# Optimization experiments

Hardware: AMD Instinct MI355X
Metric: run time of the kernel (lower is better)

Reference implementation:

```python
import jax, jax.numpy as jnp
import numpy as np

B, C, H, W = 4, 128, 128, 128
E, K, HID = 11, 6, 512  # num_experts, active_experts, 4*dim


def setup_inputs() -> dict:
    key = jax.random.key(0)
    ks = jax.random.split(key, 5)
    return {
        "x": jax.random.normal(ks[0], (B, C, H, W), jnp.float32),
        "gate_w": jax.random.normal(ks[1], (E, C), jnp.float32) * 0.02,
        "gate_b": jnp.zeros((E,), jnp.float32),
        "w1": jax.random.normal(ks[2], (E, HID, C), jnp.float32) * 0.02,
        "b1": jnp.zeros((E, HID), jnp.float32),
        "w2": jax.random.normal(ks[3], (E, C, HID), jnp.float32) * 0.02,
        "b2": jnp.zeros((E, C), jnp.float32),
    }


def reference(x, gate_w, gate_b, w1, b1, w2, b2):
    n_experts = gate_w.shape[0]
    k = K  # active_experts
    # channels-last for per-pixel routing / 1x1-conv-as-matmul
    xcl = jnp.transpose(x, (0, 2, 3, 1))  # [B,H,W,C]
    # --- router (1x1 conv gate + softmax over experts + top-k) ---
    logits = jnp.einsum('bhwc,ec->bhwe', xcl, gate_w) + gate_b
    scores = jax.nn.softmax(logits, axis=-1)            # [B,H,W,E]
    topk_p, topk_i = jax.lax.top_k(scores, k)           # [B,H,W,K]
    topk_p = topk_p / topk_p.sum(axis=-1, keepdims=True)
    # scatter routing weights into dense per-expert mask (indices distinct)
    onehot = jax.nn.one_hot(topk_i, n_experts, dtype=x.dtype)  # [B,H,W,K,E]
    mask = jnp.einsum('bhwke,bhwk->bhwe', onehot, topk_p)      # [B,H,W,E]
    # --- dense expert compute, masked accumulate (as in original loop) ---
    acc = jnp.zeros_like(xcl)
    for e in range(n_experts):
        h = jax.nn.gelu(jnp.einsum('bhwc,dc->bhwd', xcl, w1[e]) + b1[e],
                        approximate=False)  # torch GELU is exact erf form
        oe = jnp.einsum('bhwd,cd->bhwc', h, w2[e]) + b2[e]
        acc = acc + mask[..., e:e + 1] * oe
    y = x + jnp.transpose(acc, (0, 3, 1, 2))  # back to NCHW
    # --- load-balancing aux loss ---
    mean_prob = scores.mean(axis=(0, 1, 2))            # [E]
    mean_load = onehot.sum(axis=3).mean(axis=(0, 1, 2))  # binary mask mean, [E]
    aux_loss = n_experts * jnp.sum(mean_prob * mean_load)
    return (y, aux_loss)
```

## Files before the change

### kernel.cpp

```cpp
#include <hip/hip_runtime.h>
#include <stdint.h>

#define C_   128
#define HW_  16384
#define CHW_ (C_*HW_)
#define N_   65536
#define E_   11
#define K_   6
#define HID_ 512

typedef __attribute__((ext_vector_type(8))) _Float16 half8;
typedef __attribute__((ext_vector_type(2))) _Float16 h2;
typedef __attribute__((ext_vector_type(2))) __fp16 fp16v2;
typedef __attribute__((ext_vector_type(16))) float float16v;
typedef __attribute__((ext_vector_type(2))) unsigned uint2v;

#define GLD(g, s) __builtin_amdgcn_global_load_lds( \
    (const __attribute__((address_space(1))) unsigned int*)(uintptr_t)(g), \
    (__attribute__((address_space(3))) unsigned int*)(unsigned int)(uintptr_t)(s), 16, 0, 0)

__device__ __forceinline__ h2 pkrtz(float a, float b){
  union { fp16v2 f; h2 h; } u;
  u.f = __builtin_amdgcn_cvt_pkrtz(a, b);
  return u.h;
}
__device__ __forceinline__ h2 gelu2h(h2 v, h2 wr2){
  h2 u = v * v;
  h2 s = u * (h2)(_Float16)(-0.00076957f) + (h2)(_Float16)(0.0147811f);
  s = s * u + (h2)(_Float16)(-0.126434f);
  s = s * u + (h2)(_Float16)(0.795742f);
  h2 p = v * s;
  h2 phi = p * (h2)(_Float16)(0.5f) + (h2)(_Float16)(0.5f);
  return v * wr2 * phi;
}
__device__ __forceinline__ void pswap32(unsigned &a, unsigned &b){
#if __has_builtin(__builtin_amdgcn_permlane32_swap)
  uint2v r = __builtin_amdgcn_permlane32_swap(a, b, false, false);
  a = r.x; b = r.y;
#else
  asm volatile("v_permlane32_swap_b32 %0, %1" : "+v"(a), "+v"(b));
#endif
}

__global__ __launch_bounds__(256) void k_convert(const float* __restrict__ w1,
                                                 const float* __restrict__ w2,
                                                 const float* __restrict__ b1,
                                                 unsigned short* __restrict__ wimg,
                                                 unsigned short* __restrict__ b1h,
                                                 float* __restrict__ auxsum){
  int t = blockIdx.x * 256 + threadIdx.x;
  if (t < 23) auxsum[t] = 0.0f;
  if (t >= 185856) return;
  if (t >= 180224){
    int t2 = t - 180224;
    int rec = t2 >> 5, j5 = t2 & 31;
    int hi = j5 >> 4, j = j5 & 15;
    int e = rec >> 4, hc = rec & 15;
    int row = (j & 3) + 8 * (j >> 2) + 4 * hi;
    union { _Float16 h; unsigned short u; } cv;
    cv.h = (_Float16)b1[e * 512 + hc * 32 + row];
    b1h[rec * 32 + j5] = cv.u;
    return;
  }
  const float* src;
  size_t dst;
  if (t < 90112){
    int e = t >> 13, hid = (t >> 4) & 511, c8 = t & 15;
    src = w1 + (size_t)t * 8;
    int rec = e * 16 + (hid >> 5);
    int kc = c8 >> 1, half = c8 & 1;
    int l = (hid & 31) | (half << 5);
    dst = (size_t)rec * 8192 + kc * 512 + l * 8;
  } else {
    int u = t - 90112;
    int e = u >> 13, cc = (u >> 6) & 127, hd8 = u & 63;
    src = w2 + (size_t)u * 8;
    int rec = e * 16 + (hd8 >> 2);
    int kc2 = (hd8 >> 1) & 1, half = hd8 & 1, ct = cc >> 5;
    int l = (cc & 31) | (half << 5);
    dst = (size_t)rec * 8192 + 4096 + (ct * 2 + kc2) * 512 + l * 8;
  }
  float4 a = *(const float4*)src, b = *(const float4*)(src + 4);
  union { _Float16 h[8]; uint4 v; } u4;
  u4.h[0] = (_Float16)a.x; u4.h[1] = (_Float16)a.y;
  u4.h[2] = (_Float16)a.z; u4.h[3] = (_Float16)a.w;
  u4.h[4] = (_Float16)b.x; u4.h[5] = (_Float16)b.y;
  u4.h[6] = (_Float16)b.z; u4.h[7] = (_Float16)b.w;
  *(uint4*)(wimg + dst) = u4.v;
}

__global__ __launch_bounds__(512, 2) void k_ffn(const float* __restrict__ x,
                                                const float* __restrict__ gw,
                                                const float* __restrict__ gb,
                                                float* __restrict__ mask,
                                                const unsigned short* __restrict__ wimg,
                                                const unsigned short* __restrict__ b1h,
                                                const float* __restrict__ b2,
                                                float* __restrict__ auxsum,
                                                float* __restrict__ y){
  __shared__ unsigned char smem[65536];
  __shared__ int b2f;
  int tid = threadIdx.x;
  int w = tid >> 6, l = tid & 63;
  int l31 = l & 31, hi = l >> 5;
  int hi4 = hi * 4;
  int pix0 = blockIdx.x * 256;
  int off = (blockIdx.x % 11) * 16;
  const unsigned char* wimgB = (const unsigned char*)wimg;
  const unsigned char* b1hB  = (const unsigned char*)b1h;

  if (tid == 0) b2f = 0;

  half8 Xf[8];

  {
    float* tt  = (float*)smem;
    float* g   = (float*)(smem + 33280);
    float* gbs = (float*)(smem + 38912);
    float* ap  = (float*)(smem + 38976);
    float* al  = (float*)(smem + 39040);

    for (int i = tid; i < E_ * C_; i += 512) g[i] = gw[i];
    if (tid < E_){ gbs[tid] = gb[tid]; ap[tid] = 0.f; al[tid] = 0.f; }

    int myrr = w >> 1;
    #pragma unroll 1
    for (int rr = 0; rr < 4; ++rr){
      int pixc = pix0 + rr * 64;
      const float* xb = x + (size_t)(pixc >> 14) * CHW_ + (pixc & 16383);
      __syncthreads();
      #pragma unroll
      for (int it = 0; it < 4; ++it){
        int flat = it * 512 + tid;
        int c = flat >> 4, p4 = (flat & 15) << 2;
        float4 v = *(const float4*)(xb + (size_t)c * HW_ + p4);
        tt[(p4 + 0) * 130 + c] = v.x;
        tt[(p4 + 1) * 130 + c] = v.y;
        tt[(p4 + 2) * 130 + c] = v.z;
        tt[(p4 + 3) * 130 + c] = v.w;
      }
      __syncthreads();
      if (myrr == rr){
        const float2* trow = (const float2*)(tt + (32 * (w & 1) + l31) * 130 + hi * 8);
        #pragma unroll
        for (int kc = 0; kc < 8; ++kc){
          union { unsigned u[4]; half8 s; } cv;
          #pragma unroll
          for (int m = 0; m < 4; ++m){
            float2 f = trow[kc * 8 + m];
            union { h2 h; unsigned uu; } pv;
            pv.h = pkrtz(f.x, f.y);
            cv.u[m] = pv.uu;
          }
          Xf[kc] = cv.s;
        }
      }
      if (tid < 256){
        int p = tid >> 2, t4 = tid & 3;
        float lg[E_];
        #pragma unroll
        for (int e = 0; e < E_; ++e) lg[e] = (t4 == 0) ? gbs[e] : 0.f;
        const float2* ttrow = (const float2*)(tt + p * 130 + t4 * 32);
        #pragma unroll 4
        for (int j2 = 0; j2 < 16; ++j2){
          float2 xv = ttrow[j2];
          #pragma unroll
          for (int e = 0; e < E_; ++e){
            float2 gv = *(const float2*)(g + e * C_ + t4 * 32 + j2 * 2);
            lg[e] = fmaf(xv.x, gv.x, lg[e]);
            lg[e] = fmaf(xv.y, gv.y, lg[e]);
          }
        }
        #pragma unroll
        for (int e = 0; e < E_; ++e){
          lg[e] += __shfl_xor(lg[e], 1, 64);
          lg[e] += __shfl_xor(lg[e], 2, 64);
        }
        float mx = lg[0];
        #pragma unroll
        for (int e = 1; e < E_; ++e) mx = fmaxf(mx, lg[e]);
        float pr[E_]; float s = 0.f;
        #pragma unroll
        for (int e = 0; e < E_; ++e){ pr[e] = expf(lg[e] - mx); s += pr[e]; }
        float inv = 1.0f / s;
        #pragma unroll
        for (int e = 0; e < E_; ++e) pr[e] *= inv;

        unsigned selmask = 0; float wsum = 0.f;
        for (int k = 0; k < K_; ++k){
          float bv = -1.f; int bi = 0;
          #pragma unroll
          for (int e = 0; e < E_; ++e){
            bool better = (((selmask >> e) & 1u) == 0u) && (pr[e] > bv);
            bv = better ? pr[e] : bv;
            bi = better ? e : bi;
          }
          selmask |= 1u << bi; wsum += bv;
        }
        float invw = 1.0f / wsum;
        if (t4 == 0){
          int pix = pixc + p;
          #pragma unroll
          for (int e = 0; e < E_; ++e){
            bool sel = (selmask >> e) & 1u;
            mask[(size_t)pix * E_ + e] = sel ? pr[e] * invw : 0.f;
            atomicAdd(&ap[e], pr[e]);
            if (sel) atomicAdd(&al[e], 1.0f);
          }
        }
      }
    }
    __syncthreads();
    if (tid < E_){
      atomicAdd(&auxsum[tid], ap[tid]);
      atomicAdd(&auxsum[E_ + tid], al[tid]);
    }
  }

  uint4 bhA[4], bhB[4];
  const size_t mrow = (size_t)(pix0 + w * 32 + l31) * 11;

  {
    #pragma unroll
    for (int k = 0; k < 2; ++k){
      int rec = off + k;
      const unsigned char* gs = wimgB + (size_t)rec * 16384 + w * 2048 + l * 16;
      unsigned char* dst = smem + k * 16384 + w * 2048;
      GLD(gs, dst);
      GLD(gs + 1024, dst + 1024);
    }
    #pragma unroll
    for (int k = 0; k < 2; ++k){
      const unsigned char* bp = b1hB + (off + k) * 64 + hi * 32;
      bhA[2 * k]     = *(const uint4*)(bp);
      bhA[2 * k + 1] = *(const uint4*)(bp + 16);
    }
  }
  float wrn = mask[mrow + (off >> 4)];
  __syncthreads();

  float16v facc[4];
  #pragma unroll
  for (int ct = 0; ct < 4; ++ct) facc[ct] = (float16v)0.0f;
  h2 wr2 = (h2)(_Float16)0.0f;

#define REC_BODY(WB, BH0, BH1)                                                      \
  {                                                                                 \
    float16v hacc_ = (float16v)0.0f;                                                \
    _Pragma("unroll")                                                               \
    for (int kc_ = 0; kc_ < 8; ++kc_){                                              \
      half8 a_ = *(const half8*)((WB) + kc_ * 1024 + l * 16);                       \
      hacc_ = __builtin_amdgcn_mfma_f32_32x32x16_f16(a_, Xf[kc_], hacc_, 0, 0, 0);  \
    }                                                                               \
    union { uint4 v[2]; h2 h[8]; } bu_;                                             \
    bu_.v[0] = BH0; bu_.v[1] = BH1;                                                 \
    unsigned pd_[8];                                                                \
    _Pragma("unroll")                                                               \
    for (int k_ = 0; k_ < 8; ++k_){                                                 \
      h2 v_ = pkrtz(hacc_[2 * k_], hacc_[2 * k_ + 1]);                              \
      v_ = v_ + bu_.h[k_];                                                          \
      union { h2 h; unsigned u; } g_;                                               \
      g_.h = gelu2h(v_, wr2);                                                       \
      pd_[k_] = g_.u;                                                               \
    }                                                                               \
    pswap32(pd_[0], pd_[2]); pswap32(pd_[1], pd_[3]);                               \
    pswap32(pd_[4], pd_[6]); pswap32(pd_[5], pd_[7]);                               \
    union { unsigned u[4]; half8 s; } cv0_, cv1_;                                   \
    cv0_.u[0] = pd_[0]; cv0_.u[1] = pd_[1]; cv0_.u[2] = pd_[2]; cv0_.u[3] = pd_[3]; \
    cv1_.u[0] = pd_[4]; cv1_.u[1] = pd_[5]; cv1_.u[2] = pd_[6]; cv1_.u[3] = pd_[7]; \
    _Pragma("unroll")                                                               \
    for (int ct_ = 0; ct_ < 4; ++ct_){                                              \
      half8 a0_ = *(const half8*)((WB) + 8192 + (ct_ * 2 + 0) * 1024 + l * 16);     \
      half8 a1_ = *(const half8*)((WB) + 8192 + (ct_ * 2 + 1) * 1024 + l * 16);     \
      facc[ct_] = __builtin_amdgcn_mfma_f32_32x32x16_f16(a0_, cv0_.s, facc[ct_], 0, 0, 0); \
      facc[ct_] = __builtin_amdgcn_mfma_f32_32x32x16_f16(a1_, cv1_.s, facc[ct_], 0, 0, 0); \
    }                                                                               \
  }

#define SUPER_BODY(J, BHC, BHL)                                                     \
  {                                                                                 \
    asm volatile("s_waitcnt vmcnt(4)" ::: "memory");                                \
    __builtin_amdgcn_s_barrier();                                                   \
    __builtin_amdgcn_sched_barrier(0);                                              \
         \
    {                                                                               \
      unsigned char* dbuf_ = smem + ((((J) + 1) & 1) << 15);                        \
      _Pragma("unroll")                                                             \
      for (int k_ = 0; k_ < 2; ++k_){                                               \
        int rn_ = 2 * (J) + 2 + k_ + off; if (rn_ >= 176) rn_ -= 176;               \
        const unsigned char* gs_ = wimgB + (size_t)rn_ * 16384 + w * 2048 + l * 16; \
        unsigned char* dst_ = dbuf_ + k_ * 16384 + w * 2048;                        \
        GLD(gs_, dst_);                                                             \
        GLD(gs_ + 1024, dst_ + 1024);                                               \
      }                                                                             \
      __builtin_amdgcn_sched_barrier(0);                                            \
      _Pragma("unroll")                                                             \
      for (int k_ = 0; k_ < 2; ++k_){                                               \
        int rn_ = 2 * (J) + 2 + k_ + off; if (rn_ >= 176) rn_ -= 176;               \
        const unsigned char* bp_ = b1hB + rn_ * 64 + hi * 32;                       \
        BHL[2 * k_]     = *(const uint4*)(bp_);                                     \
        BHL[2 * k_ + 1] = *(const uint4*)(bp_ + 16);                                \
      }                                                                             \
    }                                                                               \
    __builtin_amdgcn_sched_barrier(0);                                              \
    if (((J) & 7) == 0){           \
      _Float16 wh_ = (_Float16)wrn;                                                 \
      wr2 = (h2){wh_, wh_};                                                         \
      int rn_ = 2 * (J) + 16 + off; if (rn_ >= 176) rn_ -= 176;                     \
      wrn = mask[mrow + (rn_ >> 4)];                                                \
    }                                                                               \
    const unsigned char* wb_ = smem + (((J) & 1) << 15);                            \
    REC_BODY(wb_, BHC[0], BHC[1]);                                                  \
    REC_BODY(wb_ + 16384, BHC[2], BHC[3]);                                          \
  }

  #pragma unroll 1
  for (int jj = 0; jj < 44; ++jj){
    SUPER_BODY(2 * jj,     bhA, bhB);
    SUPER_BODY(2 * jj + 1, bhB, bhA);
  }
#undef SUPER_BODY
#undef REC_BODY

  __syncthreads();
  float* lds_t = (float*)smem;
  float* b2t   = (float*)(smem + 17408);
  for (int idx = tid; idx < 1536; idx += 512){
    int cc = idx / 12, ee = idx - cc * 12;
    float v = (ee < 11) ? b2[ee * 128 + cc] : 0.f;
    b2t[idx] = v;
    if (v != 0.f) atomicOr(&b2f, 1);
  }
  __syncthreads();
  int b2nz = b2f;

  #pragma unroll 1
  for (int h = 0; h < 8; ++h){
    __syncthreads();
    if (w == h){
      #pragma unroll
      for (int ct = 0; ct < 4; ++ct)
        #pragma unroll
        for (int r = 0; r < 16; ++r)
          lds_t[(ct * 32 + (r & 3) + 8 * (r >> 2) + hi4) * 33 + l31] = facc[ct][r];
    }
    __syncthreads();
    int c = tid >> 2, p8 = (tid & 3) << 3;
    int pixg = pix0 + h * 32 + p8;
    size_t base = (size_t)(pixg >> 14) * CHW_ + (size_t)c * HW_ + (pixg & 16383);
    float av[8];
    #pragma unroll
    for (int k = 0; k < 8; ++k) av[k] = lds_t[c * 33 + p8 + k];
    if (b2nz){
      #pragma unroll
      for (int k = 0; k < 8; ++k){
        const float* mr = mask + (size_t)(pixg + k) * 11;
        #pragma unroll
        for (int e = 0; e < 11; ++e) av[k] = fmaf(mr[e], b2t[c * 12 + e], av[k]);
      }
    }
    float4 xv0 = *(const float4*)(x + base);
    float4 xv1 = *(const float4*)(x + base + 4);
    float4 o0 = {av[0] + xv0.x, av[1] + xv0.y, av[2] + xv0.z, av[3] + xv0.w};
    float4 o1 = {av[4] + xv1.x, av[5] + xv1.y, av[6] + xv1.z, av[7] + xv1.w};
    *(float4*)(y + base) = o0;
    *(float4*)(y + base + 4) = o1;
  }
}

__global__ __launch_bounds__(64) void k_aux(const float* __restrict__ aux,
                                            float* __restrict__ y){
  if (threadIdx.x == 0){
    float s = 0.f;
    const float invN = 1.0f / (float)N_;
    for (int e = 0; e < E_; ++e)
      s += (aux[e] * invN) * (aux[E_ + e] * invN);
    y[(size_t)N_ * C_] = (float)E_ * s;
  }
}

extern "C" void kernel_launch(void* const* d_in, const int* in_sizes, int n_in,
                              void* d_out, int out_size, void* d_ws, size_t ws_size,
                              hipStream_t stream){
  const float* x  = (const float*)d_in[0];
  const float* gw = (const float*)d_in[1];
  const float* gb = (const float*)d_in[2];
  const float* w1 = (const float*)d_in[3];
  const float* b1 = (const float*)d_in[4];
  const float* w2 = (const float*)d_in[5];
  const float* b2 = (const float*)d_in[6];
  float* y = (float*)d_out;
  char* ws = (char*)d_ws;

  unsigned short* wimg = (unsigned short*)ws;
  float* mask   = (float*)(ws + 2883584);
  float* auxsum = (float*)(ws + 5767168);
  unsigned short* b1h  = (unsigned short*)(ws + 5767264);

  hipLaunchKernelGGL(k_convert, dim3(726), dim3(256), 0, stream, w1, w2, b1, wimg, b1h, auxsum);
  hipLaunchKernelGGL(k_ffn,     dim3(256), dim3(512), 0, stream,
                     x, gw, gb, mask, wimg, b1h, b2, auxsum, y);
  hipLaunchKernelGGL(k_aux,     dim3(1),   dim3(64),  0, stream, auxsum, y);
}
```

Before: 330.0 us.

## Spread router over all threads, reduce aux atomics, fold aux kernel into last block

The gating/softmax/top-k router now uses all 512 threads (8 per pixel) instead of 256 (4 per pixel), with float4 gate weight loads and an extra shuffle stage. Per-pixel LDS atomics for the aux sums are replaced by wave-level shuffle reductions followed by one atomic per wave per expert. The separate k_aux launch is removed: a global counter makes the last-finishing block compute the aux loss, which saves one kernel launch but adds a fence and atomic per block.

Result: no change. 331.4 us (+0.4%).

```diff
diff --git a/kernel.cpp b/kernel.cpp
--- a/kernel.cpp
+++ b/kernel.cpp
@@ -49,7 +49,7 @@
                                                  unsigned short* __restrict__ b1h,
                                                  float* __restrict__ auxsum){
   int t = blockIdx.x * 256 + threadIdx.x;
-  if (t < 23) auxsum[t] = 0.0f;
+  if (t < 24) auxsum[t] = 0.0f;
   if (t >= 185856) return;
   if (t >= 180224){
     int t2 = t - 180224;
@@ -155,58 +155,63 @@
           Xf[kc] = cv.s;
         }
       }
-      if (tid < 256){
-        int p = tid >> 2, t4 = tid & 3;
+      {
+        int p = tid >> 3, t8 = tid & 7;
         float lg[E_];
         #pragma unroll
-        for (int e = 0; e < E_; ++e) lg[e] = (t4 == 0) ? gbs[e] : 0.f;
-        const float2* ttrow = (const float2*)(tt + p * 130 + t4 * 32);
-        #pragma unroll 4
-        for (int j2 = 0; j2 < 16; ++j2){
-          float2 xv = ttrow[j2];
+        for (int e = 0; e < E_; ++e) lg[e] = (t8 == 0) ? gbs[e] : 0.f;
+        const float2* ttrow = (const float2*)(tt + p * 130 + t8 * 16);
+        #pragma unroll
+        for (int j4 = 0; j4 < 4; ++j4){
+          float2 xa = ttrow[j4 * 2], xbv = ttrow[j4 * 2 + 1];
           #pragma unroll
           for (int e = 0; e < E_; ++e){
-            float2 gv = *(const float2*)(g + e * C_ + t4 * 32 + j2 * 2);
-            lg[e] = fmaf(xv.x, gv.x, lg[e]);
-            lg[e] = fmaf(xv.y, gv.y, lg[e]);
+            float4 gv = *(const float4*)(g + e * C_ + t8 * 16 + j4 * 4);
+            lg[e] = fmaf(xa.x,  gv.x, lg[e]);
+            lg[e] = fmaf(xa.y,  gv.y, lg[e]);
+            lg[e] = fmaf(xbv.x, gv.z, lg[e]);
+            lg[e] = fmaf(xbv.y, gv.w, lg[e]);
           }
         }
         #pragma unroll
         for (int e = 0; e < E_; ++e){
           lg[e] += __shfl_xor(lg[e], 1, 64);
           lg[e] += __shfl_xor(lg[e], 2, 64);
+          lg[e] += __shfl_xor(lg[e], 4, 64);
         }
         float mx = lg[0];
         #pragma unroll
         for (int e = 1; e < E_; ++e) mx = fmaxf(mx, lg[e]);
-        float pr[E_]; float s = 0.f;
-        #pragma unroll
-        for (int e = 0; e < E_; ++e){ pr[e] = expf(lg[e] - mx); s += pr[e]; }
+        float s = 0.f;
+        #pragma unroll
+        for (int e = 0; e < E_; ++e){ lg[e] = expf(lg[e] - mx); s += lg[e]; }
         float inv = 1.0f / s;
         #pragma unroll
-        for (int e = 0; e < E_; ++e) pr[e] *= inv;
-
+        for (int e = 0; e < E_; ++e) lg[e] *= inv;
         unsigned selmask = 0; float wsum = 0.f;
         for (int k = 0; k < K_; ++k){
           float bv = -1.f; int bi = 0;
           #pragma unroll
           for (int e = 0; e < E_; ++e){
-            bool better = (((selmask >> e) & 1u) == 0u) && (pr[e] > bv);
-            bv = better ? pr[e] : bv;
+            bool better = (((selmask >> e) & 1u) == 0u) && (lg[e] > bv);
+            bv = better ? lg[e] : bv;
             bi = better ? e : bi;
           }
           selmask |= 1u << bi; wsum += bv;
         }
         float invw = 1.0f / wsum;
-        if (t4 == 0){
-          int pix = pixc + p;
-          #pragma unroll
-          for (int e = 0; e < E_; ++e){
-            bool sel = (selmask >> e) & 1u;
-            mask[(size_t)pix * E_ + e] = sel ? pr[e] * invw : 0.f;
-            atomicAdd(&ap[e], pr[e]);
-            if (sel) atomicAdd(&al[e], 1.0f);
-          }
+        int pix = pixc + p;
+        #pragma unroll
+        for (int e = 0; e < E_; ++e){
+          bool sel = (selmask >> e) & 1u;
+          float pv = lg[e];
+          if (t8 == 0) mask[(size_t)pix * E_ + e] = sel ? pv * invw : 0.f;
+          float pa = (t8 == 0) ? pv : 0.f;
+          float la = (t8 == 0 && sel) ? 1.f : 0.f;
+          pa += __shfl_xor(pa, 8, 64);  la += __shfl_xor(la, 8, 64);
+          pa += __shfl_xor(pa, 16, 64); la += __shfl_xor(la, 16, 64);
+          pa += __shfl_xor(pa, 32, 64); la += __shfl_xor(la, 32, 64);
+          if (l == 0){ atomicAdd(&ap[e], pa); atomicAdd(&al[e], la); }
         }
       }
     }
@@ -214,6 +219,20 @@
     if (tid < E_){
       atomicAdd(&auxsum[tid], ap[tid]);
       atomicAdd(&auxsum[E_ + tid], al[tid]);
+    }
+    __syncthreads();
+    if (tid == 0){
+      __threadfence();
+      unsigned prev = atomicAdd((unsigned*)auxsum + 23, 1u);
+      if (prev == 255u){
+        __threadfence();
+        float s = 0.f;
+        const float invN = 1.0f / (float)N_;
+        volatile const float* va = auxsum;
+        for (int e = 0; e < E_; ++e)
+          s += (va[e] * invN) * (va[E_ + e] * invN);
+        y[(size_t)N_ * C_] = (float)E_ * s;
+      }
     }
   }
 
@@ -368,17 +387,6 @@
   }
 }
 
-__global__ __launch_bounds__(64) void k_aux(const float* __restrict__ aux,
-                                            float* __restrict__ y){
-  if (threadIdx.x == 0){
-    float s = 0.f;
-    const float invN = 1.0f / (float)N_;
-    for (int e = 0; e < E_; ++e)
-      s += (aux[e] * invN) * (aux[E_ + e] * invN);
-    y[(size_t)N_ * C_] = (float)E_ * s;
-  }
-}
-
 extern "C" void kernel_launch(void* const* d_in, const int* in_sizes, int n_in,
                               void* d_out, int out_size, void* d_ws, size_t ws_size,
                               hipStream_t stream){
@@ -400,5 +408,4 @@
   hipLaunchKernelGGL(k_convert, dim3(726), dim3(256), 0, stream, w1, w2, b1, wimg, b1h, auxsum);
   hipLaunchKernelGGL(k_ffn,     dim3(256), dim3(512), 0, stream,
                      x, gw, gb, mask, wimg, b1h, b2, auxsum, y);
-  hipLaunchKernelGGL(k_aux,     dim3(1),   dim3(64),  0, stream, auxsum, y);
-}
+}
```
